# Performance work log

Measured on AMD Instinct MI355X. Metric: run time of the kernel, lower is better.

Reference implementation:

```python
import jax, jax.numpy as jnp
import numpy as np


def setup_inputs() -> dict:
    key = jax.random.key(0)
    k1, k2, k3, k4 = jax.random.split(key, 4)
    B, T, F_in, F_out, N, E, K = 16, 64, 64, 64, 128, 2, 4
    x = jax.random.normal(k1, (B, T, F_in, N), dtype=jnp.float32)
    # graph shift operator per (batch, time, edge-feature); scaled to keep powers bounded
    S = jax.random.normal(k2, (B, T, E, N, N), dtype=jnp.float32) / np.sqrt(N)
    H = jax.random.normal(k3, (F_out, E, K, F_in), dtype=jnp.float32) * 0.02
    bias = jax.random.normal(k4, (F_out, 1), dtype=jnp.float32) * 0.02
    return {"x": x, "S": S, "H": H, "bias": bias}


def reference(x, S, H, bias):
    # x: [B,T,F_in,N], S: [B,T,E,N,N], H: [F_out,E,K,F_in], bias: [F_out,1]
    B, T, F_in, N = x.shape
    E = S.shape[2]
    F_out, _, K, _ = H.shape
    # replicate features across edge-feature dim: [B,T,E,F_in,N]
    cur = jnp.broadcast_to(x[:, :, None], (B, T, E, F_in, N))
    taps = [cur]
    zero_row = jnp.zeros((B, 1, E, F_in, N), dtype=x.dtype)
    for _ in range(1, K):
        # time-shift: tap k at time t depends on tap k-1 at time t-1
        cur = jnp.concatenate([zero_row, cur[:, :-1]], axis=1)
        # diffuse over graph: [..,F_in,N] @ [..,N,N]
        cur = jnp.matmul(cur, S)
        taps.append(cur)
    z = jnp.stack(taps, axis=2)  # [B,T,K,E,F_in,N]
    # [B,T,N, E*K*F_in], matching permute(0,1,5,3,2,4) in the source
    z = z.transpose(0, 1, 5, 3, 2, 4).reshape(B, T, N, E * K * F_in)
    Hm = H.reshape(F_out, E * K * F_in)
    y = jnp.einsum('btnf,of->bton', z, Hm)  # [B,T,F_out,N]
    return y + bias  # bias [F_out,1] broadcasts over N
```

## Files before the change

kernel.cpp:

```cpp
#include <hip/hip_runtime.h>


namespace {
constexpr int B = 16, T = 64, F = 64, N = 128, E = 2, K = 4;
constexpr int SS = 136;
}

typedef short v8s __attribute__((ext_vector_type(8)));
typedef float v4f __attribute__((ext_vector_type(4)));

__device__ inline ushort f2bf(float f) {
  union { float f; uint u; } v; v.f = f;
  uint u = v.u;
  return (ushort)((u + 0x7fffu + ((u >> 16) & 1u)) >> 16);
}

__device__ inline uint pk2(float a, float b) {
  return (uint)f2bf(a) | ((uint)f2bf(b) << 16);
}

__global__ __launch_bounds__(256) void cvt_H(const float* __restrict__ H,
                                             ushort* __restrict__ Hb) {
  const int d4 = blockIdx.x * 256 + threadIdx.x;
  const int d = d4 * 4;
  const int f = d & 63, o = (d >> 6) & 63, k = (d >> 12) & 3, e = (d >> 14) & 1;
  const float4 v = *(const float4*)(H + (((size_t)o * E + e) * K + k) * F + f);
  uint2 w;
  w.x = pk2(v.x, v.y);
  w.y = pk2(v.z, v.w);
  *(uint2*)(Hb + d) = w;
}

__global__ __launch_bounds__(256) void cvt_S(const float* __restrict__ S,
                                             ushort* __restrict__ ST) {
  __shared__ ushort tile[128 * 128];
  const int bid = blockIdx.x;
  const float* Sg = S + (size_t)bid * N * N;
  ushort* Og = ST + (size_t)bid * N * N;
  const int tid = threadIdx.x;
  #pragma unroll
  for (int it = 0; it < 8; ++it) {
    const int idx = tid + it * 256;
    const int m = idx >> 4, g = idx & 15;
    const float4 v0 = *(const float4*)(Sg + m * N + g * 8);
    const float4 v1 = *(const float4*)(Sg + m * N + g * 8 + 4);
    uint4 w;
    w.x = pk2(v0.x, v0.y); w.y = pk2(v0.z, v0.w);
    w.z = pk2(v1.x, v1.y); w.w = pk2(v1.z, v1.w);
    const int gp = g ^ (m >> 3);
    *(uint4*)&tile[m * 128 + gp * 8] = w;
  }
  __syncthreads();
  const int a = tid & 15, b = tid >> 4;
  v8s rows[8];
  #pragma unroll
  for (int j = 0; j < 8; ++j)
    rows[j] = *(const v8s*)&tile[(8 * a + j) * 128 + ((b ^ a) * 8)];
  #pragma unroll
  for (int i = 0; i < 8; ++i) {
    uint4 w;
    w.x = (uint)(ushort)rows[0][i] | ((uint)(ushort)rows[1][i] << 16);
    w.y = (uint)(ushort)rows[2][i] | ((uint)(ushort)rows[3][i] << 16);
    w.z = (uint)(ushort)rows[4][i] | ((uint)(ushort)rows[5][i] << 16);
    w.w = (uint)(ushort)rows[6][i] | ((uint)(ushort)rows[7][i] << 16);
    *(uint4*)(Og + (8 * b + i) * N + 8 * a) = w;
  }
}

__global__ __launch_bounds__(256) void cvt_X(const float* __restrict__ x,
                                             ushort* __restrict__ xT) {
  __shared__ ushort tile[64 * 128];
  const int bid = blockIdx.x;
  const float* xg = x + (size_t)bid * F * N;
  ushort* Og = xT + (size_t)bid * N * F;
  const int tid = threadIdx.x;
  #pragma unroll
  for (int it = 0; it < 4; ++it) {
    const int idx = tid + it * 256;
    const int f = idx >> 4, g = idx & 15;
    const float4 v0 = *(const float4*)(xg + f * N + g * 8);
    const float4 v1 = *(const float4*)(xg + f * N + g * 8 + 4);
    uint4 w;
    w.x = pk2(v0.x, v0.y); w.y = pk2(v0.z, v0.w);
    w.z = pk2(v1.x, v1.y); w.w = pk2(v1.z, v1.w);
    const int gp = g ^ (f >> 3);
    *(uint4*)&tile[f * 128 + gp * 8] = w;
  }
  __syncthreads();
  if (tid < 128) {
    const int a = tid & 7, b = tid >> 3;
    v8s rows[8];
    #pragma unroll
    for (int j = 0; j < 8; ++j)
      rows[j] = *(const v8s*)&tile[(8 * a + j) * 128 + ((b ^ a) * 8)];
    #pragma unroll
    for (int i = 0; i < 8; ++i) {
      uint4 w;
      w.x = (uint)(ushort)rows[0][i] | ((uint)(ushort)rows[1][i] << 16);
      w.y = (uint)(ushort)rows[2][i] | ((uint)(ushort)rows[3][i] << 16);
      w.z = (uint)(ushort)rows[4][i] | ((uint)(ushort)rows[5][i] << 16);
      w.w = (uint)(ushort)rows[6][i] | ((uint)(ushort)rows[7][i] << 16);
      *(uint4*)(Og + (8 * b + i) * F + 8 * a) = w;
    }
  }
}

__device__ inline void load_hf(const ushort* __restrict__ Hb, int e, int k,
                               int ob0, int l15, int q, v8s hf[2][2]) {
  #pragma unroll
  for (int mt = 0; mt < 2; ++mt)
    #pragma unroll
    for (int fk = 0; fk < 2; ++fk)
      hf[mt][fk] = *(const v8s*)(Hb +
          ((size_t)((e * K + k) * 64 + ob0 + 16 * mt + l15)) * 64 + fk * 32 + q * 8);
}

__device__ inline void load_xf(const ushort* __restrict__ xb,
                               int nb0, int l15, int q, v8s xf[4][2]) {
  #pragma unroll
  for (int nt = 0; nt < 4; ++nt)
    #pragma unroll
    for (int fk = 0; fk < 2; ++fk)
      xf[nt][fk] = *(const v8s*)(xb + (nb0 + 16 * nt + l15) * F + fk * 32 + q * 8);
}

__device__ inline void load_pf(const ushort* __restrict__ Pg,
                               int ob0, int l15, int q, v8s pf[2][2][2]) {
  #pragma unroll
  for (int mt = 0; mt < 2; ++mt)
    #pragma unroll
    for (int h = 0; h < 2; ++h)
      #pragma unroll
      for (int lk = 0; lk < 2; ++lk)
        pf[mt][h][lk] = *(const v8s*)(Pg +
            (ob0 + 16 * mt + l15) * N + h * 64 + lk * 32 + q * 8);
}

__device__ inline void stage_S(const ushort* __restrict__ STg, ushort* sS, int tid) {
  #pragma unroll
  for (int it = 0; it < 8; ++it) {
    const int idx = tid + it * 256;
    const int n = idx >> 4, m8 = (idx & 15) * 8;
    *(uint4*)&sS[n * SS + m8] = *(const uint4*)(STg + n * N + m8);
  }
}

__device__ inline void zero_acc(v4f acc[2][4]) {
  #pragma unroll
  for (int i = 0; i < 2; ++i)
    #pragma unroll
    for (int j = 0; j < 4; ++j) {
      acc[i][j][0] = 0.f; acc[i][j][1] = 0.f; acc[i][j][2] = 0.f; acc[i][j][3] = 0.f;
    }
}

__device__ inline void do_proj(const v8s hf[2][2], const v8s xf[4][2],
                               v4f acc[2][4]) {
  #pragma unroll
  for (int fk = 0; fk < 2; ++fk)
    #pragma unroll
    for (int mt = 0; mt < 2; ++mt)
      #pragma unroll
      for (int nt = 0; nt < 4; ++nt)
        acc[mt][nt] = __builtin_amdgcn_mfma_f32_16x16x32_bf16(
            hf[mt][fk], xf[nt][fk], acc[mt][nt], 0, 0, 0);
}

__device__ inline void do_mm(const v8s pf[2][2][2], const ushort* sS,
                             v4f acc[2][4], int nb0, int l15, int q) {
  #pragma unroll
  for (int h = 0; h < 2; ++h)
    #pragma unroll
    for (int lk = 0; lk < 2; ++lk) {
      v8s bb[4];
      #pragma unroll
      for (int nt = 0; nt < 4; ++nt)
        bb[nt] = *(const v8s*)&sS[(nb0 + 16 * nt + l15) * SS + h * 64 + lk * 32 + q * 8];
      #pragma unroll
      for (int mt = 0; mt < 2; ++mt)
        #pragma unroll
        for (int nt = 0; nt < 4; ++nt)
          acc[mt][nt] = __builtin_amdgcn_mfma_f32_16x16x32_bf16(
              pf[mt][h][lk], bb[nt], acc[mt][nt], 0, 0, 0);
    }
}

__device__ inline void store_W(ushort* __restrict__ Og, v4f acc[2][4],
                               int ob0, int nb0, int l15, int q) {
  #pragma unroll
  for (int mt = 0; mt < 2; ++mt)
    #pragma unroll
    for (int nt = 0; nt < 4; ++nt) {
      const int col = nb0 + 16 * nt + l15;
      #pragma unroll
      for (int r = 0; r < 4; ++r)
        Og[(ob0 + 16 * mt + q * 4 + r) * N + col] = f2bf(acc[mt][nt][r]);
    }
}

__global__ __launch_bounds__(256, 4) void gf_proj(
    const ushort* __restrict__ xT, const ushort* __restrict__ Hb,
    ushort* __restrict__ Out, int k) {
  const int bid = blockIdx.x;
  const int e = bid & 1, bs = bid >> 1;
  const int tid = threadIdx.x, w = tid >> 6, lane = tid & 63;
  const int l15 = lane & 15, q = lane >> 4;
  const int ob0 = (w & 1) * 32, nb0 = (w >> 1) * 64;
  v8s hf[2][2], xf[4][2];
  load_hf(Hb, e, k, ob0, l15, q, hf);
  load_xf(xT + (size_t)bs * N * F, nb0, l15, q, xf);
  v4f acc[2][4];
  zero_acc(acc);
  do_proj(hf, xf, acc);
  store_W(Out + (size_t)bid * F * N, acc, ob0, nb0, l15, q);
}

__global__ __launch_bounds__(256, 4) void gf_step(
    const ushort* __restrict__ xT, const ushort* __restrict__ ST,
    const ushort* __restrict__ Hb, const ushort* __restrict__ Pin,
    ushort* __restrict__ Out, int k) {
  __shared__ ushort sS[128 * SS];
  const int bid = blockIdx.x;
  const int e = bid & 1, bs = bid >> 1;
  const int s = bs & (T - 1);
  const int tid = threadIdx.x, w = tid >> 6, lane = tid & 63;
  const int l15 = lane & 15, q = lane >> 4;
  const int ob0 = (w & 1) * 32, nb0 = (w >> 1) * 64;
  const bool has_p = (s > 0);

  if (has_p) stage_S(ST + (size_t)bid * N * N, sS, tid);

  v8s hf[2][2], xf[4][2];
  load_hf(Hb, e, k, ob0, l15, q, hf);
  load_xf(xT + (size_t)bs * N * F, nb0, l15, q, xf);

  v4f acc[2][4];
  zero_acc(acc);
  do_proj(hf, xf, acc);

  if (has_p) {
    v8s pf[2][2][2];
    load_pf(Pin + (size_t)((bs - 1) * E + e) * F * N, ob0, l15, q, pf);
    __syncthreads();
    do_mm(pf, sS, acc, nb0, l15, q);
  }
  store_W(Out + (size_t)bid * F * N, acc, ob0, nb0, l15, q);
}

__global__ __launch_bounds__(256, 4) void gf_final(
    const ushort* __restrict__ xT, const ushort* __restrict__ ST,
    const ushort* __restrict__ Hb, const ushort* __restrict__ Pin,
    const float* __restrict__ bias, float* __restrict__ y) {
  __shared__ ushort sS[128 * SS];
  const int bid = blockIdx.x;
  const int t = bid & (T - 1);
  const int tid = threadIdx.x, w = tid >> 6, lane = tid & 63;
  const int l15 = lane & 15, q = lane >> 4;
  const int ob0 = (w & 1) * 32, nb0 = (w >> 1) * 64;
  const bool has_p = (t > 0);

  v4f acc[2][4];
  zero_acc(acc);

  #pragma unroll
  for (int e = 0; e < E; ++e) {
    if (has_p) {
      if (e > 0) __syncthreads();
      stage_S(ST + (size_t)(bid * E + e) * N * N, sS, tid);
    }
    v8s hf[2][2], xf[4][2];
    load_hf(Hb, e, 0, ob0, l15, q, hf);
    load_xf(xT + (size_t)bid * N * F, nb0, l15, q, xf);
    do_proj(hf, xf, acc);
    if (has_p) {
      v8s pf[2][2][2];
      load_pf(Pin + (size_t)((bid - 1) * E + e) * F * N, ob0, l15, q, pf);
      __syncthreads();
      do_mm(pf, sS, acc, nb0, l15, q);
    }
  }

  float* yg = y + (size_t)bid * F * N;
  #pragma unroll
  for (int mt = 0; mt < 2; ++mt)
    #pragma unroll
    for (int nt = 0; nt < 4; ++nt) {
      const int col = nb0 + 16 * nt + l15;
      #pragma unroll
      for (int r = 0; r < 4; ++r) {
        const int row = ob0 + 16 * mt + q * 4 + r;
        yg[row * N + col] = acc[mt][nt][r] + bias[row];
      }
    }
}

extern "C" void kernel_launch(void* const* d_in, const int* in_sizes, int n_in,
                              void* d_out, int out_size, void* d_ws, size_t ws_size,
                              hipStream_t stream) {
  const float* x    = (const float*)d_in[0];
  const float* S    = (const float*)d_in[1];
  const float* H    = (const float*)d_in[2];
  const float* bias = (const float*)d_in[3];
  float* y = (float*)d_out;

  const size_t STn = (size_t)B * T * E * N * N;
  const size_t XTn = (size_t)B * T * N * F;
  const size_t Wn  = (size_t)B * T * E * F * N;
  ushort* ST = (ushort*)d_ws;
  ushort* xT = ST + STn;
  ushort* Wa = xT + XTn;
  ushort* Wb = Wa + Wn;
  ushort* Hb = Wb + Wn;

  cvt_H   <<<32,        256, 0, stream>>>(H, Hb);
  cvt_X   <<<B * T,     256, 0, stream>>>(x, xT);
  cvt_S   <<<B * T * E, 256, 0, stream>>>(S, ST);
  gf_proj <<<B * T * E, 256, 0, stream>>>(xT, Hb, Wa, 3);
  gf_step <<<B * T * E, 256, 0, stream>>>(xT, ST, Hb, Wa, Wb, 2);
  gf_step <<<B * T * E, 256, 0, stream>>>(xT, ST, Hb, Wb, Wa, 1);
  gf_final<<<B * T,     256, 0, stream>>>(xT, ST, Hb, Wa, bias, y);
}
```

Baseline: 342.6 us.

## Fuse tap chain into one kernel per timestep and merge conversion kernels

The three cvt kernels become one prep launch, and the proj/step/step/final chain is replaced by a single gf_chain kernel. Each block recomputes the Horner-style tap recursion for its timestep, keeping intermediates in registers and a small per-wave LDS buffer, which removes the bf16 W intermediate round-trips through global memory and several launches. In exchange each block redoes the upstream taps for t-1..t-3, so S and x are read up to four times from global/L2. S fragments are now loaded straight from global rather than staged in LDS.

```diff
diff --git a/kernel.cpp b/kernel.cpp
--- a/kernel.cpp
+++ b/kernel.cpp
@@ -3,7 +3,7 @@
 
 namespace {
 constexpr int B = 16, T = 64, F = 64, N = 128, E = 2, K = 4;
-constexpr int SS = 136;
+constexpr int SZ = 136;
 }
 
 typedef short v8s __attribute__((ext_vector_type(8)));
@@ -19,76 +19,31 @@
   return (uint)f2bf(a) | ((uint)f2bf(b) << 16);
 }
 
-__global__ __launch_bounds__(256) void cvt_H(const float* __restrict__ H,
-                                             ushort* __restrict__ Hb) {
-  const int d4 = blockIdx.x * 256 + threadIdx.x;
-  const int d = d4 * 4;
-  const int f = d & 63, o = (d >> 6) & 63, k = (d >> 12) & 3, e = (d >> 14) & 1;
-  const float4 v = *(const float4*)(H + (((size_t)o * E + e) * K + k) * F + f);
-  uint2 w;
-  w.x = pk2(v.x, v.y);
-  w.y = pk2(v.z, v.w);
-  *(uint2*)(Hb + d) = w;
-}
-
-__global__ __launch_bounds__(256) void cvt_S(const float* __restrict__ S,
-                                             ushort* __restrict__ ST) {
+__global__ __launch_bounds__(256) void gf_prep(
+    const float* __restrict__ x, const float* __restrict__ S,
+    const float* __restrict__ H, ushort* __restrict__ xT,
+    ushort* __restrict__ ST, ushort* __restrict__ Hb) {
   __shared__ ushort tile[128 * 128];
   const int bid = blockIdx.x;
-  const float* Sg = S + (size_t)bid * N * N;
-  ushort* Og = ST + (size_t)bid * N * N;
   const int tid = threadIdx.x;
-  #pragma unroll
-  for (int it = 0; it < 8; ++it) {
-    const int idx = tid + it * 256;
-    const int m = idx >> 4, g = idx & 15;
-    const float4 v0 = *(const float4*)(Sg + m * N + g * 8);
-    const float4 v1 = *(const float4*)(Sg + m * N + g * 8 + 4);
-    uint4 w;
-    w.x = pk2(v0.x, v0.y); w.y = pk2(v0.z, v0.w);
-    w.z = pk2(v1.x, v1.y); w.w = pk2(v1.z, v1.w);
-    const int gp = g ^ (m >> 3);
-    *(uint4*)&tile[m * 128 + gp * 8] = w;
-  }
-  __syncthreads();
-  const int a = tid & 15, b = tid >> 4;
-  v8s rows[8];
-  #pragma unroll
-  for (int j = 0; j < 8; ++j)
-    rows[j] = *(const v8s*)&tile[(8 * a + j) * 128 + ((b ^ a) * 8)];
-  #pragma unroll
-  for (int i = 0; i < 8; ++i) {
-    uint4 w;
-    w.x = (uint)(ushort)rows[0][i] | ((uint)(ushort)rows[1][i] << 16);
-    w.y = (uint)(ushort)rows[2][i] | ((uint)(ushort)rows[3][i] << 16);
-    w.z = (uint)(ushort)rows[4][i] | ((uint)(ushort)rows[5][i] << 16);
-    w.w = (uint)(ushort)rows[6][i] | ((uint)(ushort)rows[7][i] << 16);
-    *(uint4*)(Og + (8 * b + i) * N + 8 * a) = w;
-  }
-}
-
-__global__ __launch_bounds__(256) void cvt_X(const float* __restrict__ x,
-                                             ushort* __restrict__ xT) {
-  __shared__ ushort tile[64 * 128];
-  const int bid = blockIdx.x;
-  const float* xg = x + (size_t)bid * F * N;
-  ushort* Og = xT + (size_t)bid * N * F;
-  const int tid = threadIdx.x;
-  #pragma unroll
-  for (int it = 0; it < 4; ++it) {
-    const int idx = tid + it * 256;
-    const int f = idx >> 4, g = idx & 15;
-    const float4 v0 = *(const float4*)(xg + f * N + g * 8);
-    const float4 v1 = *(const float4*)(xg + f * N + g * 8 + 4);
-    uint4 w;
-    w.x = pk2(v0.x, v0.y); w.y = pk2(v0.z, v0.w);
-    w.z = pk2(v1.x, v1.y); w.w = pk2(v1.z, v1.w);
-    const int gp = g ^ (f >> 3);
-    *(uint4*)&tile[f * 128 + gp * 8] = w;
-  }
-  __syncthreads();
-  if (tid < 128) {
-    const int a = tid & 7, b = tid >> 3;
+
+  if (bid < B * T * E) {
+    const float* Sg = S + (size_t)bid * N * N;
+    ushort* Og = ST + (size_t)bid * N * N;
+    #pragma unroll
+    for (int it = 0; it < 8; ++it) {
+      const int idx = tid + it * 256;
+      const int m = idx >> 4, g = idx & 15;
+      const float4 v0 = *(const float4*)(Sg + m * N + g * 8);
+      const float4 v1 = *(const float4*)(Sg + m * N + g * 8 + 4);
+      uint4 w;
+      w.x = pk2(v0.x, v0.y); w.y = pk2(v0.z, v0.w);
+      w.z = pk2(v1.x, v1.y); w.w = pk2(v1.z, v1.w);
+      const int gp = g ^ (m >> 3);
+      *(uint4*)&tile[m * 128 + gp * 8] = w;
+    }
+    __syncthreads();
+    const int a = tid & 15, b = tid >> 4;
     v8s rows[8];
     #pragma unroll
     for (int j = 0; j < 8; ++j)
@@ -100,198 +55,136 @@
       w.y = (uint)(ushort)rows[2][i] | ((uint)(ushort)rows[3][i] << 16);
       w.z = (uint)(ushort)rows[4][i] | ((uint)(ushort)rows[5][i] << 16);
       w.w = (uint)(ushort)rows[6][i] | ((uint)(ushort)rows[7][i] << 16);
-      *(uint4*)(Og + (8 * b + i) * F + 8 * a) = w;
-    }
-  }
-}
-
-__device__ inline void load_hf(const ushort* __restrict__ Hb, int e, int k,
-                               int ob0, int l15, int q, v8s hf[2][2]) {
-  #pragma unroll
-  for (int mt = 0; mt < 2; ++mt)
-    #pragma unroll
-    for (int fk = 0; fk < 2; ++fk)
-      hf[mt][fk] = *(const v8s*)(Hb +
-          ((size_t)((e * K + k) * 64 + ob0 + 16 * mt + l15)) * 64 + fk * 32 + q * 8);
-}
-
-__device__ inline void load_xf(const ushort* __restrict__ xb,
-                               int nb0, int l15, int q, v8s xf[4][2]) {
-  #pragma unroll
-  for (int nt = 0; nt < 4; ++nt)
-    #pragma unroll
-    for (int fk = 0; fk < 2; ++fk)
-      xf[nt][fk] = *(const v8s*)(xb + (nb0 + 16 * nt + l15) * F + fk * 32 + q * 8);
-}
-
-__device__ inline void load_pf(const ushort* __restrict__ Pg,
-                               int ob0, int l15, int q, v8s pf[2][2][2]) {
-  #pragma unroll
-  for (int mt = 0; mt < 2; ++mt)
-    #pragma unroll
-    for (int h = 0; h < 2; ++h)
+      *(uint4*)(Og + (8 * b + i) * N + 8 * a) = w;
+    }
+  } else if (bid < B * T * E + B * T) {
+    const int xb = bid - B * T * E;
+    const float* xg = x + (size_t)xb * F * N;
+    ushort* Og = xT + (size_t)xb * N * F;
+    #pragma unroll
+    for (int it = 0; it < 4; ++it) {
+      const int idx = tid + it * 256;
+      const int f = idx >> 4, g = idx & 15;
+      const float4 v0 = *(const float4*)(xg + f * N + g * 8);
+      const float4 v1 = *(const float4*)(xg + f * N + g * 8 + 4);
+      uint4 w;
+      w.x = pk2(v0.x, v0.y); w.y = pk2(v0.z, v0.w);
+      w.z = pk2(v1.x, v1.y); w.w = pk2(v1.z, v1.w);
+      const int gp = g ^ (f >> 3);
+      *(uint4*)&tile[f * 128 + gp * 8] = w;
+    }
+    __syncthreads();
+    if (tid < 128) {
+      const int a = tid & 7, b = tid >> 3;
+      v8s rows[8];
       #pragma unroll
-      for (int lk = 0; lk < 2; ++lk)
-        pf[mt][h][lk] = *(const v8s*)(Pg +
-            (ob0 + 16 * mt + l15) * N + h * 64 + lk * 32 + q * 8);
-}
-
-__device__ inline void stage_S(const ushort* __restrict__ STg, ushort* sS, int tid) {
-  #pragma unroll
-  for (int it = 0; it < 8; ++it) {
-    const int idx = tid + it * 256;
-    const int n = idx >> 4, m8 = (idx & 15) * 8;
-    *(uint4*)&sS[n * SS + m8] = *(const uint4*)(STg + n * N + m8);
-  }
-}
-
-__device__ inline void zero_acc(v4f acc[2][4]) {
-  #pragma unroll
-  for (int i = 0; i < 2; ++i)
-    #pragma unroll
-    for (int j = 0; j < 4; ++j) {
-      acc[i][j][0] = 0.f; acc[i][j][1] = 0.f; acc[i][j][2] = 0.f; acc[i][j][3] = 0.f;
-    }
-}
-
-__device__ inline void do_proj(const v8s hf[2][2], const v8s xf[4][2],
-                               v4f acc[2][4]) {
-  #pragma unroll
-  for (int fk = 0; fk < 2; ++fk)
-    #pragma unroll
-    for (int mt = 0; mt < 2; ++mt)
+      for (int j = 0; j < 8; ++j)
+        rows[j] = *(const v8s*)&tile[(8 * a + j) * 128 + ((b ^ a) * 8)];
       #pragma unroll
-      for (int nt = 0; nt < 4; ++nt)
-        acc[mt][nt] = __builtin_amdgcn_mfma_f32_16x16x32_bf16(
-            hf[mt][fk], xf[nt][fk], acc[mt][nt], 0, 0, 0);
-}
-
-__device__ inline void do_mm(const v8s pf[2][2][2], const ushort* sS,
-                             v4f acc[2][4], int nb0, int l15, int q) {
-  #pragma unroll
-  for (int h = 0; h < 2; ++h)
-    #pragma unroll
-    for (int lk = 0; lk < 2; ++lk) {
-      v8s bb[4];
-      #pragma unroll
-      for (int nt = 0; nt < 4; ++nt)
-        bb[nt] = *(const v8s*)&sS[(nb0 + 16 * nt + l15) * SS + h * 64 + lk * 32 + q * 8];
-      #pragma unroll
-      for (int mt = 0; mt < 2; ++mt)
-        #pragma unroll
-        for (int nt = 0; nt < 4; ++nt)
-          acc[mt][nt] = __builtin_amdgcn_mfma_f32_16x16x32_bf16(
-              pf[mt][h][lk], bb[nt], acc[mt][nt], 0, 0, 0);
-    }
-}
-
-__device__ inline void store_W(ushort* __restrict__ Og, v4f acc[2][4],
-                               int ob0, int nb0, int l15, int q) {
-  #pragma unroll
-  for (int mt = 0; mt < 2; ++mt)
-    #pragma unroll
-    for (int nt = 0; nt < 4; ++nt) {
-      const int col = nb0 + 16 * nt + l15;
-      #pragma unroll
-      for (int r = 0; r < 4; ++r)
-        Og[(ob0 + 16 * mt + q * 4 + r) * N + col] = f2bf(acc[mt][nt][r]);
-    }
-}
-
-__global__ __launch_bounds__(256, 4) void gf_proj(
-    const ushort* __restrict__ xT, const ushort* __restrict__ Hb,
-    ushort* __restrict__ Out, int k) {
-  const int bid = blockIdx.x;
-  const int e = bid & 1, bs = bid >> 1;
-  const int tid = threadIdx.x, w = tid >> 6, lane = tid & 63;
-  const int l15 = lane & 15, q = lane >> 4;
-  const int ob0 = (w & 1) * 32, nb0 = (w >> 1) * 64;
-  v8s hf[2][2], xf[4][2];
-  load_hf(Hb, e, k, ob0, l15, q, hf);
-  load_xf(xT + (size_t)bs * N * F, nb0, l15, q, xf);
-  v4f acc[2][4];
-  zero_acc(acc);
-  do_proj(hf, xf, acc);
-  store_W(Out + (size_t)bid * F * N, acc, ob0, nb0, l15, q);
-}
-
-__global__ __launch_bounds__(256, 4) void gf_step(
+      for (int i = 0; i < 8; ++i) {
+        uint4 w;
+        w.x = (uint)(ushort)rows[0][i] | ((uint)(ushort)rows[1][i] << 16);
+        w.y = (uint)(ushort)rows[2][i] | ((uint)(ushort)rows[3][i] << 16);
+        w.z = (uint)(ushort)rows[4][i] | ((uint)(ushort)rows[5][i] << 16);
+        w.w = (uint)(ushort)rows[6][i] | ((uint)(ushort)rows[7][i] << 16);
+        *(uint4*)(Og + (8 * b + i) * F + 8 * a) = w;
+      }
+    }
+  } else {
+    const int hb = bid - (B * T * E + B * T);
+    const int d = (hb * 256 + tid) * 4;
+    const int f = d & 63, o = (d >> 6) & 63, k = (d >> 12) & 3, e = (d >> 14) & 1;
+    const float4 v = *(const float4*)(H + (((size_t)o * E + e) * K + k) * F + f);
+    uint2 w;
+    w.x = pk2(v.x, v.y);
+    w.y = pk2(v.z, v.w);
+    *(uint2*)(Hb + d) = w;
+  }
+}
+
+__global__ __launch_bounds__(256, 4) void gf_chain(
     const ushort* __restrict__ xT, const ushort* __restrict__ ST,
-    const ushort* __restrict__ Hb, const ushort* __restrict__ Pin,
-    ushort* __restrict__ Out, int k) {
-  __shared__ ushort sS[128 * SS];
-  const int bid = blockIdx.x;
-  const int e = bid & 1, bs = bid >> 1;
-  const int s = bs & (T - 1);
-  const int tid = threadIdx.x, w = tid >> 6, lane = tid & 63;
-  const int l15 = lane & 15, q = lane >> 4;
-  const int ob0 = (w & 1) * 32, nb0 = (w >> 1) * 64;
-  const bool has_p = (s > 0);
-
-  if (has_p) stage_S(ST + (size_t)bid * N * N, sS, tid);
-
-  v8s hf[2][2], xf[4][2];
-  load_hf(Hb, e, k, ob0, l15, q, hf);
-  load_xf(xT + (size_t)bs * N * F, nb0, l15, q, xf);
-
-  v4f acc[2][4];
-  zero_acc(acc);
-  do_proj(hf, xf, acc);
-
-  if (has_p) {
-    v8s pf[2][2][2];
-    load_pf(Pin + (size_t)((bs - 1) * E + e) * F * N, ob0, l15, q, pf);
-    __syncthreads();
-    do_mm(pf, sS, acc, nb0, l15, q);
-  }
-  store_W(Out + (size_t)bid * F * N, acc, ob0, nb0, l15, q);
-}
-
-__global__ __launch_bounds__(256, 4) void gf_final(
-    const ushort* __restrict__ xT, const ushort* __restrict__ ST,
-    const ushort* __restrict__ Hb, const ushort* __restrict__ Pin,
-    const float* __restrict__ bias, float* __restrict__ y) {
-  __shared__ ushort sS[128 * SS];
+    const ushort* __restrict__ Hb, const float* __restrict__ bias,
+    float* __restrict__ y) {
+  __shared__ ushort sZs[4][16 * SZ];
   const int bid = blockIdx.x;
   const int t = bid & (T - 1);
   const int tid = threadIdx.x, w = tid >> 6, lane = tid & 63;
   const int l15 = lane & 15, q = lane >> 4;
-  const int ob0 = (w & 1) * 32, nb0 = (w >> 1) * 64;
-  const bool has_p = (t > 0);
-
-  v4f acc[2][4];
-  zero_acc(acc);
-
+  ushort* sZ = sZs[w];
+  const int o = w * 16 + l15;
+
+  v4f yacc[8];
   #pragma unroll
+  for (int i = 0; i < 8; ++i) {
+    yacc[i][0] = 0.f; yacc[i][1] = 0.f; yacc[i][2] = 0.f; yacc[i][3] = 0.f;
+  }
+
   for (int e = 0; e < E; ++e) {
-    if (has_p) {
-      if (e > 0) __syncthreads();
-      stage_S(ST + (size_t)(bid * E + e) * N * N, sS, tid);
-    }
-    v8s hf[2][2], xf[4][2];
-    load_hf(Hb, e, 0, ob0, l15, q, hf);
-    load_xf(xT + (size_t)bid * N * F, nb0, l15, q, xf);
-    do_proj(hf, xf, acc);
-    if (has_p) {
-      v8s pf[2][2][2];
-      load_pf(Pin + (size_t)((bid - 1) * E + e) * F * N, ob0, l15, q, pf);
-      __syncthreads();
-      do_mm(pf, sS, acc, nb0, l15, q);
-    }
-  }
-
-  float* yg = y + (size_t)bid * F * N;
+    v4f acc[8];
+    bool have = false;
+    #pragma unroll
+    for (int tap = 3; tap >= 0; --tap) {
+      const int s = t - tap;
+      if (s < 0) continue;
+      const bool doMM = have;
+      if (doMM) {
+        __builtin_amdgcn_wave_barrier();
+        #pragma unroll
+        for (int mt = 0; mt < 8; ++mt) {
+          uint2 wv;
+          wv.x = pk2(acc[mt][0], acc[mt][1]);
+          wv.y = pk2(acc[mt][2], acc[mt][3]);
+          *(uint2*)&sZ[l15 * SZ + mt * 16 + q * 4] = wv;
+        }
+        __builtin_amdgcn_wave_barrier();
+      }
+      v4f* const tgt = (tap == 0) ? yacc : acc;
+      if (tap != 0) {
+        #pragma unroll
+        for (int mt = 0; mt < 8; ++mt) {
+          tgt[mt][0] = 0.f; tgt[mt][1] = 0.f; tgt[mt][2] = 0.f; tgt[mt][3] = 0.f;
+        }
+      }
+      if (doMM) {
+        const ushort* Sg = ST + ((size_t)(bid - tap) * E + e) * (N * N);
+        #pragma unroll
+        for (int c = 0; c < 4; ++c) {
+          const v8s bz = *(const v8s*)&sZ[l15 * SZ + c * 32 + q * 8];
+          #pragma unroll
+          for (int mt = 0; mt < 8; ++mt) {
+            const v8s af = *(const v8s*)(Sg + (mt * 16 + l15) * N + c * 32 + q * 8);
+            tgt[mt] = __builtin_amdgcn_mfma_f32_16x16x32_bf16(af, bz, tgt[mt], 0, 0, 0);
+          }
+        }
+      }
+      {
+        const ushort* hrow = Hb + ((size_t)((e * K + tap) * 64) + o) * 64;
+        const v8s bh0 = *(const v8s*)(hrow + q * 8);
+        const v8s bh1 = *(const v8s*)(hrow + 32 + q * 8);
+        const ushort* xrow = xT + (size_t)(bid - tap) * (N * F);
+        #pragma unroll
+        for (int mt = 0; mt < 8; ++mt) {
+          const ushort* xr = xrow + (mt * 16 + l15) * F;
+          const v8s ax0 = *(const v8s*)(xr + q * 8);
+          const v8s ax1 = *(const v8s*)(xr + 32 + q * 8);
+          tgt[mt] = __builtin_amdgcn_mfma_f32_16x16x32_bf16(ax0, bh0, tgt[mt], 0, 0, 0);
+          tgt[mt] = __builtin_amdgcn_mfma_f32_16x16x32_bf16(ax1, bh1, tgt[mt], 0, 0, 0);
+        }
+      }
+      have = true;
+    }
+  }
+
+  const float bv = bias[o];
+  float* yg = y + (size_t)bid * F * N + (size_t)o * N;
   #pragma unroll
-  for (int mt = 0; mt < 2; ++mt)
-    #pragma unroll
-    for (int nt = 0; nt < 4; ++nt) {
-      const int col = nb0 + 16 * nt + l15;
-      #pragma unroll
-      for (int r = 0; r < 4; ++r) {
-        const int row = ob0 + 16 * mt + q * 4 + r;
-        yg[row * N + col] = acc[mt][nt][r] + bias[row];
-      }
-    }
+  for (int mt = 0; mt < 8; ++mt) {
+    float4 v;
+    v.x = yacc[mt][0] + bv; v.y = yacc[mt][1] + bv;
+    v.z = yacc[mt][2] + bv; v.w = yacc[mt][3] + bv;
+    *(float4*)(yg + mt * 16 + q * 4) = v;
+  }
 }
 
 extern "C" void kernel_launch(void* const* d_in, const int* in_sizes, int n_in,
@@ -305,18 +198,10 @@
 
   const size_t STn = (size_t)B * T * E * N * N;
   const size_t XTn = (size_t)B * T * N * F;
-  const size_t Wn  = (size_t)B * T * E * F * N;
   ushort* ST = (ushort*)d_ws;
   ushort* xT = ST + STn;
-  ushort* Wa = xT + XTn;
-  ushort* Wb = Wa + Wn;
-  ushort* Hb = Wb + Wn;
-
-  cvt_H   <<<32,        256, 0, stream>>>(H, Hb);
-  cvt_X   <<<B * T,     256, 0, stream>>>(x, xT);
-  cvt_S   <<<B * T * E, 256, 0, stream>>>(S, ST);
-  gf_proj <<<B * T * E, 256, 0, stream>>>(xT, Hb, Wa, 3);
-  gf_step <<<B * T * E, 256, 0, stream>>>(xT, ST, Hb, Wa, Wb, 2);
-  gf_step <<<B * T * E, 256, 0, stream>>>(xT, ST, Hb, Wb, Wa, 1);
-  gf_final<<<B * T,     256, 0, stream>>>(xT, ST, Hb, Wa, bias, y);
-}
+  ushort* Hb = xT + XTn;
+
+  gf_prep <<<B * T * E + B * T + 32, 256, 0, stream>>>(x, S, H, xT, ST, Hb);
+  gf_chain<<<B * T,                  256, 0, stream>>>(xT, ST, Hb, bias, y);
+}
```

After: 455.3 us. +32.9%, slower.
